# Kernel optimization log

Measured on AMD Instinct MI355X. Metric: run time of the kernel, lower is better.

Reference implementation:

```python
import jax, jax.numpy as jnp
import numpy as np

LOG2PI = float(np.log(2.0 * np.pi))
BATCH = 131072
IN_FEATURES = 128
MULT = 3          # Gaussian multiplicity / Sum in_channels
CARD = 2          # first Product cardinality -> 64 features


def setup_inputs() -> dict:
    key = jax.random.key(0)
    k1, k2, k3, k4, k5 = jax.random.split(key, 5)
    x = jax.random.normal(k1, (BATCH, IN_FEATURES), dtype=jnp.float32)
    means = jax.random.normal(k2, (1, IN_FEATURES, MULT), dtype=jnp.float32)
    # stds drawn positive (torch.rand init for scale params)
    stds = jax.random.uniform(k3, (1, IN_FEATURES, MULT), dtype=jnp.float32,
                              minval=0.1, maxval=1.0)
    sum_weights = jax.random.normal(k4, (64, MULT, 1), dtype=jnp.float32)
    # randomized Product layer: fixed random permutation of the 128 features
    perm = jax.random.permutation(k5, IN_FEATURES).astype(jnp.int32)
    return {"x": x, "means": means, "stds": stds,
            "sum_weights": sum_weights, "perm": perm}


def reference(x, means, stds, sum_weights, perm):
    n = x.shape[0]
    # --- Gaussian leaf: Normal(mu, sigma).log_prob(x) -> [n, 128, 3]
    z = (x[:, :, None] - means) / stds
    lp = -0.5 * (z * z) - jnp.log(stds) - 0.5 * LOG2PI
    # --- Product(in_features=128, cardinality=2, randomize): permute features,
    # pair them up, product in log-domain = sum -> [n, 64, 3]
    lp = lp[:, perm, :]
    lp = lp.reshape(n, IN_FEATURES // CARD, CARD, MULT).sum(axis=2)
    # --- Sum(in_channels=3, in_features=64, out_channels=1): weighted
    # log-sum-exp mixture over channels with log_softmax-normalized weights
    logw = jax.nn.log_softmax(sum_weights, axis=1)          # [64, 3, 1]
    lp = jax.nn.logsumexp(lp[:, :, :, None] + logw[None], axis=2)  # [n, 64, 1]
    # --- Product(in_features=64, cardinality=64): sum all features -> [n, 1, 1]
    # (permutation before a full reduction is a no-op, so omitted)
    out = lp.sum(axis=1, keepdims=True).reshape(n, 1, 1)
    return out
```

## Files before the change

### kernel.cpp

```cpp
#include <hip/hip_runtime.h>

#define N_FEAT 128
#define ROWS   32
#define TPB    256

__global__ __launch_bounds__(TPB)
void spn_fused(const float* __restrict__ x,
               const float* __restrict__ means,
               const float* __restrict__ stds,
               const float* __restrict__ sumw,
               const int* __restrict__ perm,
               float* __restrict__ out, int n) {
    __shared__ float sx[ROWS * N_FEAT];
    __shared__ float snm0[192], sis0[192], snm1[192], sis1[192], sC2[192];
    __shared__ int   sp0[64], sp1[64];

    const float NHALF_LOG2E = -0.7213475204444817f;
    const float LN2 = 0.6931471805599453f;

    const int tid  = threadIdx.x;
    const int lane = tid & 63;
    const int wv   = tid >> 6;

    if (tid < 64) {
        const float LOG2PI_ = 1.8378770664093453f;
        const float LOG2E   = 1.4426950408889634f;
        const int g  = tid;
        const int p0 = perm[2 * g], p1 = perm[2 * g + 1];
        sp0[g] = p0; sp1[g] = p1;
        float w0 = sumw[g * 3 + 0], w1 = sumw[g * 3 + 1], w2 = sumw[g * 3 + 2];
        float mx  = fmaxf(w0, fmaxf(w1, w2));
        float lse = mx + logf(expf(w0 - mx) + expf(w1 - mx) + expf(w2 - mx));
#pragma unroll
        for (int m = 0; m < 3; ++m) {
            float s0 = stds[p0 * 3 + m], mu0 = means[p0 * 3 + m];
            float s1 = stds[p1 * 3 + m], mu1 = means[p1 * 3 + m];
            float i0 = 1.0f / s0, i1 = 1.0f / s1;
            float lw = sumw[g * 3 + m] - lse;
            snm0[g * 3 + m] = mu0 * i0;
            sis0[g * 3 + m] = i0;
            snm1[g * 3 + m] = mu1 * i1;
            sis1[g * 3 + m] = i1;
            sC2[g * 3 + m]  = (lw - logf(s0) - logf(s1) - LOG2PI_) * LOG2E;
        }
    }
    __syncthreads();

    const int p0 = sp0[lane];
    const int p1 = sp1[lane];
    float nm0[3], is0[3], nm1[3], is1[3], C2[3];
#pragma unroll
    for (int m = 0; m < 3; ++m) {
        nm0[m] = snm0[lane * 3 + m];
        is0[m] = sis0[lane * 3 + m];
        nm1[m] = snm1[lane * 3 + m];
        is1[m] = sis1[lane * 3 + m];
        C2[m]  = sC2[lane * 3 + m];
    }

    const int ntiles = n / ROWS;
    for (int tile = blockIdx.x; tile < ntiles; tile += gridDim.x) {
        const int rowbase = tile * ROWS;
        __syncthreads();

        const float4* xv = (const float4*)(x + (size_t)rowbase * N_FEAT);
        float4* sv = (float4*)sx;
#pragma unroll
        for (int it = 0; it < 4; ++it)
            sv[it * TPB + tid] = xv[it * TPB + tid];
        __syncthreads();

        float res[8];
#pragma unroll
        for (int r = 0; r < 8; ++r) {
            const float* xr = sx + (wv * 8 + r) * N_FEAT;
            const float a = xr[p0];
            const float b = xr[p1];
            float v0, v1, v2;
            {
                float z0 = fmaf(a, is0[0], -nm0[0]);
                float z1 = fmaf(b, is1[0], -nm1[0]);
                v0 = fmaf(z0 * z0, NHALF_LOG2E, C2[0]);
                v0 = fmaf(z1 * z1, NHALF_LOG2E, v0);
            }
            {
                float z0 = fmaf(a, is0[1], -nm0[1]);
                float z1 = fmaf(b, is1[1], -nm1[1]);
                v1 = fmaf(z0 * z0, NHALF_LOG2E, C2[1]);
                v1 = fmaf(z1 * z1, NHALF_LOG2E, v1);
            }
            {
                float z0 = fmaf(a, is0[2], -nm0[2]);
                float z1 = fmaf(b, is1[2], -nm1[2]);
                v2 = fmaf(z0 * z0, NHALF_LOG2E, C2[2]);
                v2 = fmaf(z1 * z1, NHALF_LOG2E, v2);
            }
            float mx = fmaxf(v0, fmaxf(v1, v2));
            float s = __builtin_amdgcn_exp2f(v0 - mx)
                    + __builtin_amdgcn_exp2f(v1 - mx)
                    + __builtin_amdgcn_exp2f(v2 - mx);
            res[r] = mx + __builtin_amdgcn_logf(s);
        }

#pragma unroll
        for (int off = 32; off >= 1; off >>= 1) {
#pragma unroll
            for (int r = 0; r < 8; ++r)
                res[r] += __shfl_xor(res[r], off, 64);
        }

        if (lane == 0) {
#pragma unroll
            for (int r = 0; r < 8; ++r)
                out[rowbase + wv * 8 + r] = res[r] * LN2;
        }
    }
}

extern "C" void kernel_launch(void* const* d_in, const int* in_sizes, int n_in,
                              void* d_out, int out_size, void* d_ws, size_t ws_size,
                              hipStream_t stream) {
    const float* x     = (const float*)d_in[0];
    const float* means = (const float*)d_in[1];
    const float* stds  = (const float*)d_in[2];
    const float* sumw  = (const float*)d_in[3];
    const int*   perm  = (const int*)d_in[4];
    float* out = (float*)d_out;
    int n = in_sizes[0] / N_FEAT;

    hipLaunchKernelGGL(spn_fused, dim3(1024), dim3(TPB), 0, stream,
                       x, means, stds, sumw, perm, out, n);
}
```

Measured before the change: 101.6 us.

## Load x tiles via async global-to-LDS DMA and use DPP wave reductions

New measurement: 104.9 us. 1.03x slower.

```diff
diff --git a/kernel.cpp b/kernel.cpp
--- a/kernel.cpp
+++ b/kernel.cpp
@@ -4,7 +4,33 @@
 #define ROWS   32
 #define TPB    256
 
-__global__ __launch_bounds__(TPB)
+template<int CTRL>
+__device__ __forceinline__ float dpp_xadd(float v) {
+    int t = __builtin_amdgcn_update_dpp(0, __float_as_int(v), CTRL, 0xF, 0xF, true);
+    return v + __int_as_float(t);
+}
+
+__device__ __forceinline__ float wave_allsum(float v) {
+    v = dpp_xadd<0xB1>(v);
+    v = dpp_xadd<0x4E>(v);
+    v = dpp_xadd<0x141>(v);
+    v = dpp_xadd<0x140>(v);
+#if __has_builtin(__builtin_amdgcn_permlane16_swap)
+    {
+        auto p = __builtin_amdgcn_permlane16_swap(__float_as_uint(v), __float_as_uint(v), false, false);
+        v = __uint_as_float(p[0]) + __uint_as_float(p[1]);
+    }
+#else
+    v += __int_as_float(__builtin_amdgcn_ds_swizzle(__float_as_int(v), 0x401F));
+#endif
+    {
+        auto p = __builtin_amdgcn_permlane32_swap(__float_as_uint(v), __float_as_uint(v), false, false);
+        v = __uint_as_float(p[0]) + __uint_as_float(p[1]);
+    }
+    return v;
+}
+
+__global__ __launch_bounds__(TPB, 6)
 void spn_fused(const float* __restrict__ x,
                const float* __restrict__ means,
                const float* __restrict__ stds,
@@ -12,64 +38,55 @@
                const int* __restrict__ perm,
                float* __restrict__ out, int n) {
     __shared__ float sx[ROWS * N_FEAT];
-    __shared__ float snm0[192], sis0[192], snm1[192], sis1[192], sC2[192];
-    __shared__ int   sp0[64], sp1[64];
 
     const float NHALF_LOG2E = -0.7213475204444817f;
-    const float LN2 = 0.6931471805599453f;
+    const float LN2     = 0.6931471805599453f;
+    const float LOG2PI_ = 1.8378770664093453f;
+    const float LOG2E   = 1.4426950408889634f;
 
     const int tid  = threadIdx.x;
     const int lane = tid & 63;
     const int wv   = tid >> 6;
 
-    if (tid < 64) {
-        const float LOG2PI_ = 1.8378770664093453f;
-        const float LOG2E   = 1.4426950408889634f;
-        const int g  = tid;
-        const int p0 = perm[2 * g], p1 = perm[2 * g + 1];
-        sp0[g] = p0; sp1[g] = p1;
-        float w0 = sumw[g * 3 + 0], w1 = sumw[g * 3 + 1], w2 = sumw[g * 3 + 2];
-        float mx  = fmaxf(w0, fmaxf(w1, w2));
-        float lse = mx + logf(expf(w0 - mx) + expf(w1 - mx) + expf(w2 - mx));
+    const int ntiles = n / ROWS;
+
+    auto issue_tile = [&](int t) {
+        const float* g0 = x + (size_t)t * (ROWS * N_FEAT);
 #pragma unroll
-        for (int m = 0; m < 3; ++m) {
-            float s0 = stds[p0 * 3 + m], mu0 = means[p0 * 3 + m];
-            float s1 = stds[p1 * 3 + m], mu1 = means[p1 * 3 + m];
-            float i0 = 1.0f / s0, i1 = 1.0f / s1;
-            float lw = sumw[g * 3 + m] - lse;
-            snm0[g * 3 + m] = mu0 * i0;
-            sis0[g * 3 + m] = i0;
-            snm1[g * 3 + m] = mu1 * i1;
-            sis1[g * 3 + m] = i1;
-            sC2[g * 3 + m]  = (lw - logf(s0) - logf(s1) - LOG2PI_) * LOG2E;
+        for (int it = 0; it < 4; ++it) {
+            const int chunk = it * 4 + wv;
+            __builtin_amdgcn_global_load_lds(
+                (const __attribute__((address_space(1))) unsigned*)(g0 + chunk * 256 + lane * 4),
+                (__attribute__((address_space(3))) unsigned*)(sx + chunk * 256),
+                16, 0, 0);
         }
-    }
-    __syncthreads();
+    };
 
-    const int p0 = sp0[lane];
-    const int p1 = sp1[lane];
+    int tile  = blockIdx.x;
+    bool have = tile < ntiles;
+    if (have) issue_tile(tile);
+
+    const int g  = lane;
+    const int p0 = perm[2 * g], p1 = perm[2 * g + 1];
+    const float w0 = sumw[g * 3 + 0], w1 = sumw[g * 3 + 1], w2 = sumw[g * 3 + 2];
+    const float wmx = fmaxf(w0, fmaxf(w1, w2));
+    const float lse = wmx + logf(expf(w0 - wmx) + expf(w1 - wmx) + expf(w2 - wmx));
     float nm0[3], is0[3], nm1[3], is1[3], C2[3];
 #pragma unroll
     for (int m = 0; m < 3; ++m) {
-        nm0[m] = snm0[lane * 3 + m];
-        is0[m] = sis0[lane * 3 + m];
-        nm1[m] = snm1[lane * 3 + m];
-        is1[m] = sis1[lane * 3 + m];
-        C2[m]  = sC2[lane * 3 + m];
+        const float s0 = stds[p0 * 3 + m], mu0 = means[p0 * 3 + m];
+        const float s1 = stds[p1 * 3 + m], mu1 = means[p1 * 3 + m];
+        const float i0 = 1.0f / s0, i1 = 1.0f / s1;
+        const float wm = (m == 0 ? w0 : (m == 1 ? w1 : w2));
+        nm0[m] = mu0 * i0;  is0[m] = i0;
+        nm1[m] = mu1 * i1;  is1[m] = i1;
+        C2[m]  = ((wm - lse) - logf(s0) - logf(s1) - LOG2PI_) * LOG2E;
     }
 
-    const int ntiles = n / ROWS;
-    for (int tile = blockIdx.x; tile < ntiles; tile += gridDim.x) {
-        const int rowbase = tile * ROWS;
+    while (have) {
         __syncthreads();
 
-        const float4* xv = (const float4*)(x + (size_t)rowbase * N_FEAT);
-        float4* sv = (float4*)sx;
-#pragma unroll
-        for (int it = 0; it < 4; ++it)
-            sv[it * TPB + tid] = xv[it * TPB + tid];
-        __syncthreads();
-
+        const int rowbase = tile * ROWS;
         float res[8];
 #pragma unroll
         for (int r = 0; r < 8; ++r) {
@@ -95,25 +112,30 @@
                 v2 = fmaf(z0 * z0, NHALF_LOG2E, C2[2]);
                 v2 = fmaf(z1 * z1, NHALF_LOG2E, v2);
             }
-            float mx = fmaxf(v0, fmaxf(v1, v2));
-            float s = __builtin_amdgcn_exp2f(v0 - mx)
-                    + __builtin_amdgcn_exp2f(v1 - mx)
-                    + __builtin_amdgcn_exp2f(v2 - mx);
-            res[r] = mx + __builtin_amdgcn_logf(s);
+            float pmx = fmaxf(v0, fmaxf(v1, v2));
+            float s = __builtin_amdgcn_exp2f(v0 - pmx)
+                    + __builtin_amdgcn_exp2f(v1 - pmx)
+                    + __builtin_amdgcn_exp2f(v2 - pmx);
+            res[r] = pmx + __builtin_amdgcn_logf(s);
         }
 
 #pragma unroll
-        for (int off = 32; off >= 1; off >>= 1) {
-#pragma unroll
-            for (int r = 0; r < 8; ++r)
-                res[r] += __shfl_xor(res[r], off, 64);
+        for (int r = 0; r < 8; ++r)
+            res[r] = wave_allsum(res[r]);
+
+        const int next = tile + (int)gridDim.x;
+        have = next < ntiles;
+        if (have) {
+            __syncthreads();
+            issue_tile(next);
         }
 
         if (lane == 0) {
-#pragma unroll
-            for (int r = 0; r < 8; ++r)
-                out[rowbase + wv * 8 + r] = res[r] * LN2;
+            float4* op = (float4*)(out + rowbase + wv * 8);
+            op[0] = make_float4(res[0] * LN2, res[1] * LN2, res[2] * LN2, res[3] * LN2);
+            op[1] = make_float4(res[4] * LN2, res[5] * LN2, res[6] * LN2, res[7] * LN2);
         }
+        tile = next;
     }
 }
 
@@ -128,6 +150,10 @@
     float* out = (float*)d_out;
     int n = in_sizes[0] / N_FEAT;
 
-    hipLaunchKernelGGL(spn_fused, dim3(1024), dim3(TPB), 0, stream,
+    int ntiles = n / ROWS;
+    int grid = ntiles > 0 ? ntiles : 1;
+    if (grid > 16384) grid = 16384;
+
+    hipLaunchKernelGGL(spn_fused, dim3(grid), dim3(TPB), 0, stream,
                        x, means, stds, sumw, perm, out, n);
 }
```
